# Kernel optimization log

Measured on AMD Instinct MI355X. Metric: run time of the kernel, lower is better.

Reference implementation:

```python
import jax, jax.numpy as jnp
import numpy as np

N, E, E_LG, H, KGE, NUM_GRAPHS, N_ITER = 100000, 500000, 1000000, 128, 128, 1024, 2
EPS = 1e-5

def _prelu(x, a):
    return jnp.where(x >= 0, x, a * x)

def _seg_mean(vals, idx, num):
    s = jax.ops.segment_sum(vals, idx, num_segments=num)
    c = jax.ops.segment_sum(jnp.ones((vals.shape[0],), vals.dtype), idx, num_segments=num)
    return s / jnp.maximum(c, 1.0)[:, None]

def setup_inputs() -> dict:
    key = jax.random.key(0)
    ks = jax.random.split(key, 16)
    sc = 1.0 / np.sqrt(H)
    inp = {
        "x": jax.random.normal(ks[0], (N, H), jnp.float32),
        "edge_attr": jax.random.normal(ks[1], (E, H), jnp.float32),
        "edge_index": jax.random.randint(ks[2], (2, E), 0, N),
        "batch": jnp.sort(jax.random.randint(ks[3], (N,), 0, NUM_GRAPHS)),
        "line_graph_edge_index": jax.random.randint(ks[4], (2, E_LG), 0, E),
        # edge_update_net: Linear + PReLU + BatchNorm1d (eval mode)
        "W1": jax.random.normal(ks[5], (H, H), jnp.float32) * sc,
        "b1": jnp.zeros((H,), jnp.float32),
        "a1": jnp.full((1,), 0.25, jnp.float32),
        "bn_gamma": jnp.ones((H,), jnp.float32),
        "bn_beta": jnp.zeros((H,), jnp.float32),
        "bn_mean": jnp.zeros((H,), jnp.float32),
        "bn_var": jnp.ones((H,), jnp.float32),
        # GRU (single layer, single step)
        "w_ih": jax.random.normal(ks[6], (3 * H, H), jnp.float32) * sc,
        "w_hh": jax.random.normal(ks[7], (3 * H, H), jnp.float32) * sc,
        "b_ih": jnp.zeros((3 * H,), jnp.float32),
        "b_hh": jnp.zeros((3 * H,), jnp.float32),
        # DynamicAttention net
        "Wa1": jax.random.normal(ks[8], (H // 2, H), jnp.float32) * sc,
        "ba1": jnp.zeros((H // 2,), jnp.float32),
        "a2": jnp.full((1,), 0.25, jnp.float32),
        "Wa2": jax.random.normal(ks[9], (1, H // 2), jnp.float32) * (1.0 / np.sqrt(H // 2)),
        "ba2": jnp.zeros((1,), jnp.float32),
        # readout
        "Wr": jax.random.normal(ks[10], (KGE, H), jnp.float32) * sc,
        "br": jnp.zeros((KGE,), jnp.float32),
    }
    return inp

def reference(x, edge_attr, W1, b1, a1, bn_gamma, bn_beta, bn_mean, bn_var,
              w_ih, w_hh, b_ih, b_hh, Wa1, ba1, a2, Wa2, ba2, Wr, br,
              edge_index, batch, line_graph_edge_index):
    src, dst = edge_index[0], edge_index[1]
    l_src, l_dst = line_graph_edge_index[0], line_graph_edge_index[1]
    h = x  # GRU hidden state [N, H]
    for _ in range(N_ITER):
        # edge-to-edge message passing (node_to_edge_proj is Identity here)
        fused = edge_attr + (x[src] + x[dst]) * 0.5  # [E, H]
        agg = _seg_mean(fused[l_src], l_dst, E)      # scatter-mean over line graph
        upd = _prelu(agg @ W1.T + b1, a1)
        upd = (upd - bn_mean) * jax.lax.rsqrt(bn_var + EPS) * bn_gamma + bn_beta
        fused = fused + upd
        node_updates = _seg_mean(fused, dst, N)      # [N, H]
        # single GRU step
        gi = node_updates @ w_ih.T + b_ih
        gh = h @ w_hh.T + b_hh
        gi_r, gi_z, gi_n = jnp.split(gi, 3, axis=-1)
        gh_r, gh_z, gh_n = jnp.split(gh, 3, axis=-1)
        r = jax.nn.sigmoid(gi_r + gh_r)
        z = jax.nn.sigmoid(gi_z + gh_z)
        n = jnp.tanh(gi_n + r * gh_n)
        h = (1.0 - z) * n + z * h
        x = h
    # dynamic attention: per-graph scalar gate
    graph_repr = _seg_mean(x, batch, NUM_GRAPHS)     # [G, H]
    attn = jax.nn.sigmoid(_prelu(graph_repr @ Wa1.T + ba1, a2) @ Wa2.T + ba2)  # [G, 1]
    attended = x * attn[batch]
    graph_emb = jax.ops.segment_sum(attended, batch, num_segments=NUM_GRAPHS)
    graph_emb = graph_emb @ Wr.T + br
    return (x, graph_emb)
```

## Files before the change

### kernel.cpp

```cpp
#include <hip/hip_runtime.h>
#include <stdint.h>

#define H 128
#define G_NUM 1024
#define BN_EPS 1e-5f

typedef unsigned int uint;
typedef unsigned short ushort;
typedef __attribute__((ext_vector_type(8))) __bf16 bf16x8;
typedef __attribute__((ext_vector_type(8))) ushort ushort8;
typedef __attribute__((ext_vector_type(4))) float f32x4;
typedef __attribute__((ext_vector_type(2))) float f32x2;

__device__ __forceinline__ float b2f(ushort u){ return __uint_as_float(((uint)u) << 16); }
__device__ __forceinline__ ushort f2b(float f){
    uint u = __float_as_uint(f);
    u += 0x7FFFu + ((u >> 16) & 1u);
    return (ushort)(u >> 16);
}
__device__ __forceinline__ float ldf(const void* p, size_t i, int bf){
    return bf ? b2f(((const ushort*)p)[i]) : ((const float*)p)[i];
}
__device__ __forceinline__ int swz(int r, int byte_in_row){
    return (r * 256 + byte_in_row) ^ ((r & 7) << 4);
}

__global__ void k_setup_small(const uint* __restrict__ gamma_bits,
                              const void* b1, const void* a1, const void* gam, const void* bet,
                              const void* mean, const void* var, const void* bih, const void* bhh,
                              float* __restrict__ ep, float* __restrict__ bi, float* __restrict__ bh,
                              int* __restrict__ flag, ushort* __restrict__ fz1, ushort* __restrict__ fz2,
                              size_t zoff, int* __restrict__ off_cat, int nk_idx, int sent_val){
    __shared__ int bfs;
    int t = threadIdx.x;
    if (t == 0){
        int f = (gamma_bits[0] == 0x3F803F80u) ? 1 : 0;
        *flag = f; bfs = f;
        off_cat[nk_idx] = sent_val;
    }
    __syncthreads();
    int bf = bfs;
    bi[t] = ldf(bih, t, bf);
    bh[t] = ldf(bhh, t, bf);
    if (t < 128){
        ep[t]       = ldf(b1, t, bf);
        ep[128 + t] = rsqrtf(ldf(var, t, bf) + BN_EPS) * ldf(gam, t, bf);
        ep[256 + t] = ldf(mean, t, bf);
        ep[384 + t] = ldf(bet, t, bf);
        fz1[zoff + t] = 0; fz2[zoff + t] = 0;
    }
    if (t == 0) ep[512] = ldf(a1, 0, bf);
}

__global__ __launch_bounds__(256) void k_count2(const int* __restrict__ lgi, const int* __restrict__ ei,
                                                int* __restrict__ cnt, int ELG, int E){
    int t = blockIdx.x * 256 + threadIdx.x;
    if (t < ELG) atomicAdd(&cnt[lgi[ELG + t]], 1);
    else { int t2 = t - ELG; if (t2 < E) atomicAdd(&cnt[E + ei[E + t2]], 1); }
}
__global__ __launch_bounds__(256) void k_scan_reduce(const int* __restrict__ cnt, int* __restrict__ bsum, int n){
    int base = blockIdx.x * 1024;
    int s = 0;
    for (int i = threadIdx.x; i < 1024; i += 256){ int idx = base + i; s += (idx < n) ? cnt[idx] : 0; }
    __shared__ int r[256];
    r[threadIdx.x] = s; __syncthreads();
    for (int o = 128; o > 0; o >>= 1){ if (threadIdx.x < o) r[threadIdx.x] += r[threadIdx.x + o]; __syncthreads(); }
    if (threadIdx.x == 0) bsum[blockIdx.x] = r[0];
}
__global__ __launch_bounds__(256) void k_scan_mid(int* __restrict__ bsum, int nb){
    __shared__ int ts[256];
    int tid = threadIdx.x;
    int loc[4]; int s = 0;
    #pragma unroll
    for (int j = 0; j < 4; j++){
        int idx = tid * 4 + j;
        loc[j] = s;
        s += (idx < nb) ? bsum[idx] : 0;
    }
    ts[tid] = s; __syncthreads();
    for (int o = 1; o < 256; o <<= 1){
        int v = (tid >= o) ? ts[tid - o] : 0;
        __syncthreads();
        ts[tid] += v;
        __syncthreads();
    }
    int texcl = ts[tid] - s;
    #pragma unroll
    for (int j = 0; j < 4; j++){
        int idx = tid * 4 + j;
        if (idx < nb) bsum[idx] = texcl + loc[j];
    }
}
__global__ __launch_bounds__(256) void k_scan_final(const int* __restrict__ cnt, const int* __restrict__ bsum,
                                                    int* __restrict__ off, int n){
    __shared__ int ts[256];
    int base = blockIdx.x * 1024;
    int tid = threadIdx.x;
    int loc[4]; int s = 0;
    #pragma unroll
    for (int j = 0; j < 4; j++){
        int idx = base + tid * 4 + j;
        loc[j] = s;
        s += (idx < n) ? cnt[idx] : 0;
    }
    ts[tid] = s; __syncthreads();
    for (int o = 1; o < 256; o <<= 1){
        int v = (tid >= o) ? ts[tid - o] : 0;
        __syncthreads();
        ts[tid] += v;
        __syncthreads();
    }
    int texcl = ts[tid] - s + bsum[blockIdx.x];
    #pragma unroll
    for (int j = 0; j < 4; j++){
        int idx = base + tid * 4 + j;
        if (idx < n) off[idx] = texcl + loc[j];
    }
}
__global__ __launch_bounds__(256) void k_fill2(const int* __restrict__ lgi, const int* __restrict__ ei,
                                               const int* __restrict__ off, int* __restrict__ cur,
                                               int* __restrict__ list, int ELG, int E){
    int t = blockIdx.x * 256 + threadIdx.x;
    if (t < ELG){
        int k = lgi[ELG + t];
        int pos = atomicAdd(&cur[k], 1);
        list[off[k] + pos] = lgi[t];
    } else {
        int t2 = t - ELG;
        if (t2 < E){
            int k = E + ei[E + t2];
            int pos = atomicAdd(&cur[k], 1);
            list[off[k] + pos] = t2;
        }
    }
}
__global__ __launch_bounds__(256) void k_cvt_bf(const void* __restrict__ in, ushort* __restrict__ out,
                                                int n, const int* __restrict__ flag){
    int t = blockIdx.x * 256 + threadIdx.x;
    if (t >= n) return;
    if (*flag) out[t] = ((const ushort*)in)[t];
    else       out[t] = f2b(((const float*)in)[t]);
}
__global__ __launch_bounds__(256) void k_wcvt(const void* __restrict__ W1, const void* __restrict__ wih,
                                              const void* __restrict__ whh, const void* __restrict__ Wr,
                                              ushort* __restrict__ W1bf, ushort* __restrict__ wihbf,
                                              ushort* __restrict__ whhbf, float* __restrict__ WrT,
                                              const int* __restrict__ flag){
    int t = blockIdx.x * 256 + threadIdx.x;
    int bf = *flag;
    if (t < 16384) W1bf[t] = bf ? ((const ushort*)W1)[t] : f2b(((const float*)W1)[t]);
    else if (t < 65536){ int i = t - 16384; wihbf[i] = bf ? ((const ushort*)wih)[i] : f2b(((const float*)wih)[i]); }
    else if (t < 114688){ int i = t - 65536; whhbf[i] = bf ? ((const ushort*)whh)[i] : f2b(((const float*)whh)[i]); }
    else if (t < 131072){ int i = t - 114688; int r = i >> 7, c = i & 127; WrT[c * 128 + r] = ldf(Wr, i, bf); }
}
__global__ __launch_bounds__(256) void k_store_h(const ushort* __restrict__ hb, void* __restrict__ out,
                                                 int n, const int* __restrict__ flag){
    int t = blockIdx.x * 256 + threadIdx.x;
    if (t >= n) return;
    ushort v = hb[t];
    if (*flag) ((ushort*)out)[t] = v;
    else       ((float*) out)[t] = b2f(v);
}

__global__ __launch_bounds__(256) void k_fused(const void* __restrict__ ea, const ushort* __restrict__ hb,
                                               const int* __restrict__ ei, ushort* __restrict__ fused,
                                               int E, const int* __restrict__ flag){
    int t = blockIdx.x * 256 + threadIdx.x;
    if (t >= E * 16) return;
    int bf = *flag;
    int e = t >> 4, ch = (t & 15) * 8;
    int s = ei[e], d = ei[E + e];
    ushort8 hs = *(const ushort8*)(hb + (size_t)s * H + ch);
    ushort8 hd = *(const ushort8*)(hb + (size_t)d * H + ch);
    size_t base = (size_t)e * H + ch;
    float av[8];
    if (bf){
        ushort8 a = *(const ushort8*)((const ushort*)ea + base);
        #pragma unroll
        for (int j = 0; j < 8; j++) av[j] = b2f(a[j]);
    } else {
        float4 a0 = *(const float4*)((const float*)ea + base);
        float4 a1 = *(const float4*)((const float*)ea + base + 4);
        av[0] = a0.x; av[1] = a0.y; av[2] = a0.z; av[3] = a0.w;
        av[4] = a1.x; av[5] = a1.y; av[6] = a1.z; av[7] = a1.w;
    }
    ushort8 o;
    #pragma unroll
    for (int j = 0; j < 8; j++) o[j] = f2b(av[j] + 0.5f * (b2f(hs[j]) + b2f(hd[j])));
    *(ushort8*)(fused + base) = o;
}

__global__ __launch_bounds__(256) void k_agg_gemm(const ushort* __restrict__ fused,
                                                  const int* __restrict__ off_cat, const int* __restrict__ list,
                                                  const ushort* __restrict__ W1bf, const float* __restrict__ ep,
                                                  ushort* __restrict__ fused2, int E, int LMAX){
    __shared__ __attribute__((aligned(16))) char As[32 * 256];
    __shared__ int offL[33];
    int tid = threadIdx.x, wid = tid >> 6, lane = tid & 63;
    int r0 = blockIdx.x * 32;
    if (tid < 33) offL[tid] = off_cat[r0 + tid];
    __syncthreads();
    int l16 = lane >> 4, ch16 = lane & 15;
    int rA = wid * 8 + l16, rB = rA + 4;
    int baseA = offL[rA], degA = offL[rA + 1] - baseA;
    int baseB = offL[rB], degB = offL[rB + 1] - baseB;
    int dm = max(degA, degB);
    #pragma unroll
    for (int o = 32; o > 0; o >>= 1) dm = max(dm, __shfl_xor(dm, o));
    f32x2 accA[4] = {}, accB[4] = {};
    #pragma unroll 2
    for (int i = 0; i < dm; i++){
        int liA = baseA + i; liA = (liA < LMAX) ? liA : (LMAX - 1);
        int liB = baseB + i; liB = (liB < LMAX) ? liB : (LMAX - 1);
        int sA = list[liA];
        int sB = list[liB];
        sA = (i < degA) ? sA : E;
        sB = (i < degB) ? sB : E;
        uint4 wA = *(const uint4*)(fused + (size_t)sA * H + ch16 * 8);
        uint4 wB = *(const uint4*)(fused + (size_t)sB * H + ch16 * 8);
        uint wa[4] = {wA.x, wA.y, wA.z, wA.w};
        uint wb[4] = {wB.x, wB.y, wB.z, wB.w};
        #pragma unroll
        for (int k2 = 0; k2 < 4; k2++){
            f32x2 va, vb;
            va.x = __uint_as_float(wa[k2] << 16); va.y = __uint_as_float(wa[k2] & 0xFFFF0000u);
            vb.x = __uint_as_float(wb[k2] << 16); vb.y = __uint_as_float(wb[k2] & 0xFFFF0000u);
            accA[k2] += va; accB[k2] += vb;
        }
    }
    float invA = 1.f / fmaxf((float)degA, 1.f);
    float invB = 1.f / fmaxf((float)degB, 1.f);
    ushort8 oA, oB;
    #pragma unroll
    for (int k2 = 0; k2 < 4; k2++){
        oA[2 * k2] = f2b(accA[k2].x * invA); oA[2 * k2 + 1] = f2b(accA[k2].y * invA);
        oB[2 * k2] = f2b(accB[k2].x * invB); oB[2 * k2 + 1] = f2b(accB[k2].y * invB);
    }
    *(ushort8*)(As + swz(rA, ch16 * 16)) = oA;
    *(ushort8*)(As + swz(rB, ch16 * 16)) = oB;
    __syncthreads();
    int lrow = lane & 15, lhi = lane >> 4;
    f32x4 acc[2][2] = {};
    #pragma unroll
    for (int ks = 0; ks < 4; ks++){
        bf16x8 afr[2];
        #pragma unroll
        for (int rt = 0; rt < 2; rt++)
            afr[rt] = *(const bf16x8*)(As + swz(rt * 16 + lrow, ks * 64 + lhi * 16));
        #pragma unroll
        for (int cc = 0; cc < 2; cc++){
            int c = (2 * wid + cc) * 16 + lrow;
            bf16x8 bfr = *(const bf16x8*)(W1bf + (size_t)c * H + ks * 32 + lhi * 8);
            #pragma unroll
            for (int rt = 0; rt < 2; rt++)
                acc[cc][rt] = __builtin_amdgcn_mfma_f32_16x16x32_bf16(afr[rt], bfr, acc[cc][rt], 0, 0, 0);
        }
    }
    __syncthreads();
    float aa = ep[512];
    #pragma unroll
    for (int cc = 0; cc < 2; cc++){
        int c = (2 * wid + cc) * 16 + lrow;
        float bb = ep[c], sc = ep[128 + c], mb = ep[256 + c], be = ep[384 + c];
        #pragma unroll
        for (int rt = 0; rt < 2; rt++)
            #pragma unroll
            for (int rg = 0; rg < 4; rg++){
                int r = rt * 16 + lhi * 4 + rg;
                float u = acc[cc][rt][rg] + bb;
                u = (u >= 0.f) ? u : aa * u;
                u = (u - mb) * sc + be;
                *(ushort*)(As + swz(r, c * 2)) = f2b(u);
            }
    }
    __syncthreads();
    #pragma unroll
    for (int q = 0; q < 2; q++){
        int r = (q == 0) ? rA : rB;
        size_t gbase = (size_t)(r0 + r) * H + ch16 * 8;
        ushort8 f = *(const ushort8*)(fused + gbase);
        ushort8 u = *(const ushort8*)(As + swz(r, ch16 * 16));
        ushort8 o;
        #pragma unroll
        for (int j = 0; j < 8; j++) o[j] = f2b(b2f(f[j]) + b2f(u[j]));
        *(ushort8*)(fused2 + gbase) = o;
    }
}

__global__ __launch_bounds__(256) void k_gru(const ushort* __restrict__ fused2,
                                             const int* __restrict__ off_cat, const int* __restrict__ list,
                                             ushort* __restrict__ hb,
                                             const ushort* __restrict__ wihbf, const ushort* __restrict__ whhbf,
                                             const float* __restrict__ bi, const float* __restrict__ bh,
                                             int N, int EZ, int LMAX){
    __shared__ __attribute__((aligned(16))) char NUs[32 * 256];
    __shared__ __attribute__((aligned(16))) char HHs[32 * 256];
    __shared__ int offL[33];
    int tid = threadIdx.x, wid = tid >> 6, lane = tid & 63;
    int r0 = blockIdx.x * 32;
    if (tid < 33) offL[tid] = off_cat[r0 + tid];
    int l16 = lane >> 4, ch16 = lane & 15;
    int rA = wid * 8 + l16, rB = rA + 4;
    *(ushort8*)(HHs + swz(rA, ch16 * 16)) = *(const ushort8*)(hb + (size_t)(r0 + rA) * H + ch16 * 8);
    *(ushort8*)(HHs + swz(rB, ch16 * 16)) = *(const ushort8*)(hb + (size_t)(r0 + rB) * H + ch16 * 8);
    __syncthreads();
    int baseA = offL[rA], degA = offL[rA + 1] - baseA;
    int baseB = offL[rB], degB = offL[rB + 1] - baseB;
    int dm = max(degA, degB);
    #pragma unroll
    for (int o = 32; o > 0; o >>= 1) dm = max(dm, __shfl_xor(dm, o));
    f32x2 accA[4] = {}, accB[4] = {};
    #pragma unroll 2
    for (int i = 0; i < dm; i++){
        int liA = baseA + i; liA = (liA < LMAX) ? liA : (LMAX - 1);
        int liB = baseB + i; liB = (liB < LMAX) ? liB : (LMAX - 1);
        int sA = list[liA];
        int sB = list[liB];
        sA = (i < degA) ? sA : EZ;
        sB = (i < degB) ? sB : EZ;
        uint4 wA = *(const uint4*)(fused2 + (size_t)sA * H + ch16 * 8);
        uint4 wB = *(const uint4*)(fused2 + (size_t)sB * H + ch16 * 8);
        uint wa[4] = {wA.x, wA.y, wA.z, wA.w};
        uint wb[4] = {wB.x, wB.y, wB.z, wB.w};
        #pragma unroll
        for (int k2 = 0; k2 < 4; k2++){
            f32x2 va, vb;
            va.x = __uint_as_float(wa[k2] << 16); va.y = __uint_as_float(wa[k2] & 0xFFFF0000u);
            vb.x = __uint_as_float(wb[k2] << 16); vb.y = __uint_as_float(wb[k2] & 0xFFFF0000u);
            accA[k2] += va; accB[k2] += vb;
        }
    }
    float invA = 1.f / fmaxf((float)degA, 1.f);
    float invB = 1.f / fmaxf((float)degB, 1.f);
    ushort8 oA, oB;
    #pragma unroll
    for (int k2 = 0; k2 < 4; k2++){
        oA[2 * k2] = f2b(accA[k2].x * invA); oA[2 * k2 + 1] = f2b(accA[k2].y * invA);
        oB[2 * k2] = f2b(accB[k2].x * invB); oB[2 * k2 + 1] = f2b(accB[k2].y * invB);
    }
    *(ushort8*)(NUs + swz(rA, ch16 * 16)) = oA;
    *(ushort8*)(NUs + swz(rB, ch16 * 16)) = oB;
    __syncthreads();
    int lrow = lane & 15, lhi = lane >> 4;
    ushort hnew[2][2][4];
    #pragma unroll
    for (int b = 0; b < 2; b++){
        f32x4 aI[3][2] = {}, aH[3][2] = {};
        #pragma unroll
        for (int ks = 0; ks < 4; ks++){
            bf16x8 fN[2], fH[2];
            #pragma unroll
            for (int rt = 0; rt < 2; rt++){
                int addr = swz(rt * 16 + lrow, ks * 64 + lhi * 16);
                fN[rt] = *(const bf16x8*)(NUs + addr);
                fH[rt] = *(const bf16x8*)(HHs + addr);
            }
            #pragma unroll
            for (int g = 0; g < 3; g++){
                int c = g * 128 + (wid + 4 * b) * 16 + lrow;
                bf16x8 bI = *(const bf16x8*)(wihbf + (size_t)c * H + ks * 32 + lhi * 8);
                bf16x8 bH = *(const bf16x8*)(whhbf + (size_t)c * H + ks * 32 + lhi * 8);
                #pragma unroll
                for (int rt = 0; rt < 2; rt++){
                    aI[g][rt] = __builtin_amdgcn_mfma_f32_16x16x32_bf16(fN[rt], bI, aI[g][rt], 0, 0, 0);
                    aH[g][rt] = __builtin_amdgcn_mfma_f32_16x16x32_bf16(fH[rt], bH, aH[g][rt], 0, 0, 0);
                }
            }
        }
        int c = (wid + 4 * b) * 16 + lrow;
        float bir = bi[c], biz = bi[128 + c], bin = bi[256 + c];
        float bhr = bh[c], bhz = bh[128 + c], bhn = bh[256 + c];
        #pragma unroll
        for (int rt = 0; rt < 2; rt++)
            #pragma unroll
            for (int rg = 0; rg < 4; rg++){
                int r = rt * 16 + lhi * 4 + rg;
                float gr = aI[0][rt][rg] + bir + aH[0][rt][rg] + bhr;
                float gz = aI[1][rt][rg] + biz + aH[1][rt][rg] + bhz;
                float rv = 1.f / (1.f + __expf(-gr));
                float zv = 1.f / (1.f + __expf(-gz));
                float nv = tanhf(aI[2][rt][rg] + bin + rv * (aH[2][rt][rg] + bhn));
                float hold = b2f(*(const ushort*)(HHs + swz(r, c * 2)));
                hnew[b][rt][rg] = f2b((1.f - zv) * nv + zv * hold);
            }
    }
    __syncthreads();
    #pragma unroll
    for (int b = 0; b < 2; b++){
        int c = (wid + 4 * b) * 16 + lrow;
        #pragma unroll
        for (int rt = 0; rt < 2; rt++)
            #pragma unroll
            for (int rg = 0; rg < 4; rg++){
                int r = rt * 16 + lhi * 4 + rg;
                *(ushort*)(NUs + swz(r, c * 2)) = hnew[b][rt][rg];
            }
    }
    __syncthreads();
    *(ushort8*)(hb + (size_t)(r0 + rA) * H + ch16 * 8) = *(const ushort8*)(NUs + swz(rA, ch16 * 16));
    *(ushort8*)(hb + (size_t)(r0 + rB) * H + ch16 * 8) = *(const ushort8*)(NUs + swz(rB, ch16 * 16));
}

__global__ __launch_bounds__(256) void k_gbounds(const int* __restrict__ batch, int* __restrict__ gs, int N, int G){
    int g = blockIdx.x * 256 + threadIdx.x;
    if (g > G) return;
    int lo = 0, hi = N;
    while (lo < hi){ int mid = (lo + hi) >> 1; if (batch[mid] < g) lo = mid + 1; else hi = mid; }
    gs[g] = lo;
}
__global__ __launch_bounds__(256) void k_graph_sum(const ushort* __restrict__ hb, const int* __restrict__ gs,
                                                   float* __restrict__ gsum){
    int g = blockIdx.x, c = threadIdx.x & 127, half = threadIdx.x >> 7;
    int s = gs[g], e = gs[g + 1];
    float acc0 = 0.f, acc1 = 0.f;
    int r = s + half;
    for (; r + 2 < e; r += 4){
        acc0 += b2f(hb[(size_t)r * H + c]);
        acc1 += b2f(hb[(size_t)(r + 2) * H + c]);
    }
    for (; r < e; r += 2) acc0 += b2f(hb[(size_t)r * H + c]);
    __shared__ float tmp[128];
    if (half == 1) tmp[c] = acc0 + acc1;
    __syncthreads();
    if (half == 0) gsum[(size_t)g * H + c] = acc0 + acc1 + tmp[c];
}
__global__ void k_attn(const float* __restrict__ gsum, const int* __restrict__ gs,
                       const void* __restrict__ Wa1, const void* __restrict__ ba1,
                       const void* __restrict__ a2, const void* __restrict__ Wa2,
                       const void* __restrict__ ba2, float* __restrict__ attn, const int* __restrict__ flag){
    int g = blockIdx.x;
    int j = threadIdx.x;
    int bf = *flag;
    float inv = 1.0f / fmaxf((float)(gs[g + 1] - gs[g]), 1.0f);
    __shared__ float R[H];
    for (int i = j; i < H; i += 64) R[i] = gsum[(size_t)g * H + i] * inv;
    __syncthreads();
    float t = 0.f;
    for (int k = 0; k < H; k++) t += R[k] * ldf(Wa1, (size_t)j * H + k, bf);
    t += ldf(ba1, j, bf);
    float al = ldf(a2, 0, bf);
    t = (t >= 0.f) ? t : al * t;
    float p = t * ldf(Wa2, j, bf);
    #pragma unroll
    for (int o = 32; o > 0; o >>= 1) p += __shfl_down(p, o);
    if (j == 0) attn[g] = 1.f / (1.f + __expf(-(p + ldf(ba2, 0, bf))));
}
__global__ __launch_bounds__(256) void k_graph_gemm(const float* __restrict__ gsum, const float* __restrict__ attn,
                                                    const float* __restrict__ WrT,
                                                    const void* __restrict__ br, void* __restrict__ out,
                                                    size_t obase, const int* __restrict__ flag){
    __shared__ float A[8 * H];
    int bf = *flag;
    int r0 = blockIdx.x * 8;
    for (int i = threadIdx.x; i < 8 * H; i += 256){
        int r = i >> 7;
        A[i] = gsum[(size_t)(r0 + r) * H + (i & 127)] * attn[r0 + r];
    }
    __syncthreads();
    int c = threadIdx.x & 127;
    int rr = (threadIdx.x >> 7) * 4;
    float acc[4] = {0, 0, 0, 0};
    for (int k = 0; k < H; k++){
        float w = WrT[k * H + c];
        #pragma unroll
        for (int j = 0; j < 4; j++) acc[j] += A[(rr + j) * H + k] * w;
    }
    float bb = ldf(br, c, bf);
    for (int j = 0; j < 4; j++){
        size_t idx = obase + (size_t)(r0 + rr + j) * H + c;
        float v = acc[j] + bb;
        if (bf) ((ushort*)out)[idx] = f2b(v);
        else    ((float*) out)[idx] = v;
    }
}

extern "C" void kernel_launch(void* const* d_in, const int* in_sizes, int n_in,
                              void* d_out, int out_size, void* d_ws, size_t ws_size,
                              hipStream_t stream)
{
    const void* x    = d_in[0];
    const void* ea   = d_in[1];
    const int*  ei   = (const int*)d_in[2];
    const int*  batch= (const int*)d_in[3];
    const int*  lgi  = (const int*)d_in[4];
    const void* W1   = d_in[5];
    const void* b1   = d_in[6];
    const void* a1   = d_in[7];
    const void* bng  = d_in[8];
    const void* bnb  = d_in[9];
    const void* bnm  = d_in[10];
    const void* bnv  = d_in[11];
    const void* wih  = d_in[12];
    const void* whh  = d_in[13];
    const void* bih  = d_in[14];
    const void* bhh  = d_in[15];
    const void* Wa1  = d_in[16];
    const void* ba1  = d_in[17];
    const void* a2   = d_in[18];
    const void* Wa2  = d_in[19];
    const void* ba2  = d_in[20];
    const void* Wr   = d_in[21];
    const void* br   = d_in[22];

    const int N   = in_sizes[0] / H;
    const int E   = in_sizes[1] / H;
    const int ELG = in_sizes[4] / 2;
    const int G   = G_NUM;
    const int NK  = E + N;
    const int nb  = (NK + 1023) / 1024;

    char* ws = (char*)d_ws;
    size_t off = 0;
    auto alloc = [&](size_t b) -> void* { void* p = ws + off; off += (b + 255) & ~(size_t)255; return p; };
    int*    flag    = (int*)   alloc(256);
    ushort* hb      = (ushort*)alloc((size_t)N * H * 2);
    ushort* fused   = (ushort*)alloc((size_t)(E + 1) * H * 2);
    ushort* fused2  = (ushort*)alloc((size_t)(E + 1) * H * 2);
    int*    zreg    = (int*)   alloc((size_t)(2 * NK) * 4);
    int*    cnt_cat = zreg;
    int*    cur_cat = zreg + NK;
    int*    off_cat = (int*)   alloc((size_t)(NK + 1) * 4);
    int*    list_cat= (int*)   alloc((size_t)(ELG + E) * 4);
    int*    bsum    = (int*)   alloc((size_t)(nb + 8) * 4);
    int*    gs      = (int*)   alloc((size_t)(G + 1) * 4);
    ushort* W1bf    = (ushort*)alloc(128 * 128 * 2);
    ushort* wihbf   = (ushort*)alloc(384 * 128 * 2);
    ushort* whhbf   = (ushort*)alloc(384 * 128 * 2);
    float*  ep      = (float*) alloc(513 * 4);
    float*  bi      = (float*) alloc(384 * 4);
    float*  bh      = (float*) alloc(384 * 4);
    float*  WrT     = (float*) alloc(128 * 128 * 4);
    float*  gsum    = (float*) alloc((size_t)G * H * 4);
    float*  attn    = (float*) alloc((size_t)G * 4);

    k_setup_small<<<1, 384, 0, stream>>>((const uint*)bng, b1, a1, bng, bnb, bnm, bnv, bih, bhh,
                                         ep, bi, bh, flag, fused, fused2, (size_t)E * H,
                                         off_cat, NK, ELG + E);

    hipMemsetAsync(zreg, 0, (size_t)(2 * NK) * 4, stream);
    k_count2<<<(ELG + E + 255) / 256, 256, 0, stream>>>(lgi, ei, cnt_cat, ELG, E);
    k_scan_reduce<<<nb, 256, 0, stream>>>(cnt_cat, bsum, NK);
    k_scan_mid<<<1, 256, 0, stream>>>(bsum, nb);
    k_scan_final<<<nb, 256, 0, stream>>>(cnt_cat, bsum, off_cat, NK);
    k_fill2<<<(ELG + E + 255) / 256, 256, 0, stream>>>(lgi, ei, off_cat, cur_cat, list_cat, ELG, E);

    k_wcvt<<<(131072 + 255) / 256, 256, 0, stream>>>(W1, wih, whh, Wr, W1bf, wihbf, whhbf, WrT, flag);

    k_cvt_bf<<<(N * H + 255) / 256, 256, 0, stream>>>(x, hb, N * H, flag);

    for (int it = 0; it < 2; it++){
        k_fused<<<(E * 16 + 255) / 256, 256, 0, stream>>>(ea, hb, ei, fused, E, flag);
        k_agg_gemm<<<(E + 31) / 32, 256, 0, stream>>>(fused, off_cat, list_cat, W1bf, ep, fused2, E, ELG);
        k_gru<<<(N + 31) / 32, 256, 0, stream>>>(fused2, off_cat + E, list_cat, hb, wihbf, whhbf, bi, bh, N, E, ELG + E);
    }

    k_gbounds<<<(G + 256) / 256, 256, 0, stream>>>(batch, gs, N, G);
    k_graph_sum<<<G, 256, 0, stream>>>(hb, gs, gsum);
    k_attn<<<G, 64, 0, stream>>>(gsum, gs, Wa1, ba1, a2, Wa2, ba2, attn, flag);
    k_graph_gemm<<<G / 8, 256, 0, stream>>>(gsum, attn, WrT, br, d_out, (size_t)N * H, flag);
    k_store_h<<<(N * H + 255) / 256, 256, 0, stream>>>(hb, d_out, N * H, flag);
}
```

Before: 965.4 us.

## Degree-sort rows within tiles to balance gather loops; fuse h store into graph sum

A new kernel bitonic-sorts each 32-row tile by in-degree into a byte permutation. The aggregation and GRU kernels use it so each wave handles rows of similar degree, which shrinks the wasted iterations from the per-wave max-degree loop. The GRU epilogue now writes new hidden values into a dedicated shared buffer, dropping one barrier and a register array. The separate final pass that stores h to the output is folded into the per-graph sum kernel, saving a full read of h. The costs are a small extra kernel, more shared memory in the GRU kernel, and an indirection load per row.

```diff
diff --git a/kernel.cpp b/kernel.cpp
--- a/kernel.cpp
+++ b/kernel.cpp
@@ -7,6 +7,7 @@
 
 typedef unsigned int uint;
 typedef unsigned short ushort;
+typedef unsigned char uchar;
 typedef __attribute__((ext_vector_type(8))) __bf16 bf16x8;
 typedef __attribute__((ext_vector_type(8))) ushort ushort8;
 typedef __attribute__((ext_vector_type(4))) float f32x4;
@@ -134,6 +135,29 @@
         }
     }
 }
+__global__ __launch_bounds__(256) void k_sortperm(const int* __restrict__ off, uchar* __restrict__ perm, int NK){
+    int t = blockIdx.x * 256 + threadIdx.x;
+    int wave = t >> 6;
+    int l = t & 63;
+    int l5 = l & 31;
+    int r0 = wave * 32;
+    if (r0 >= NK) return;
+    int r = r0 + l5;
+    int deg = off[r + 1] - off[r];
+    int key = (deg << 5) | l5;
+    #pragma unroll
+    for (int k = 2; k <= 32; k <<= 1){
+        #pragma unroll
+        for (int j = k >> 1; j > 0; j >>= 1){
+            int other = __shfl_xor(key, j);
+            bool dir = ((l5 & k) == 0);
+            bool lower = ((l5 & j) == 0);
+            int mn = min(key, other), mx = max(key, other);
+            key = (dir == lower) ? mn : mx;
+        }
+    }
+    if (l < 32) perm[r0 + l5] = (uchar)(key & 31);
+}
 __global__ __launch_bounds__(256) void k_cvt_bf(const void* __restrict__ in, ushort* __restrict__ out,
                                                 int n, const int* __restrict__ flag){
     int t = blockIdx.x * 256 + threadIdx.x;
@@ -152,14 +176,6 @@
     else if (t < 65536){ int i = t - 16384; wihbf[i] = bf ? ((const ushort*)wih)[i] : f2b(((const float*)wih)[i]); }
     else if (t < 114688){ int i = t - 65536; whhbf[i] = bf ? ((const ushort*)whh)[i] : f2b(((const float*)whh)[i]); }
     else if (t < 131072){ int i = t - 114688; int r = i >> 7, c = i & 127; WrT[c * 128 + r] = ldf(Wr, i, bf); }
-}
-__global__ __launch_bounds__(256) void k_store_h(const ushort* __restrict__ hb, void* __restrict__ out,
-                                                 int n, const int* __restrict__ flag){
-    int t = blockIdx.x * 256 + threadIdx.x;
-    if (t >= n) return;
-    ushort v = hb[t];
-    if (*flag) ((ushort*)out)[t] = v;
-    else       ((float*) out)[t] = b2f(v);
 }
 
 __global__ __launch_bounds__(256) void k_fused(const void* __restrict__ ea, const ushort* __restrict__ hb,
@@ -192,6 +208,7 @@
 
 __global__ __launch_bounds__(256) void k_agg_gemm(const ushort* __restrict__ fused,
                                                   const int* __restrict__ off_cat, const int* __restrict__ list,
+                                                  const uchar* __restrict__ perm,
                                                   const ushort* __restrict__ W1bf, const float* __restrict__ ep,
                                                   ushort* __restrict__ fused2, int E, int LMAX){
     __shared__ __attribute__((aligned(16))) char As[32 * 256];
@@ -202,8 +219,9 @@
     __syncthreads();
     int l16 = lane >> 4, ch16 = lane & 15;
     int rA = wid * 8 + l16, rB = rA + 4;
-    int baseA = offL[rA], degA = offL[rA + 1] - baseA;
-    int baseB = offL[rB], degB = offL[rB + 1] - baseB;
+    int plA = perm[r0 + rA], plB = perm[r0 + rB];
+    int baseA = offL[plA], degA = offL[plA + 1] - baseA;
+    int baseB = offL[plB], degB = offL[plB + 1] - baseB;
     int dm = max(degA, degB);
     #pragma unroll
     for (int o = 32; o > 0; o >>= 1) dm = max(dm, __shfl_xor(dm, o));
@@ -236,8 +254,8 @@
         oA[2 * k2] = f2b(accA[k2].x * invA); oA[2 * k2 + 1] = f2b(accA[k2].y * invA);
         oB[2 * k2] = f2b(accB[k2].x * invB); oB[2 * k2 + 1] = f2b(accB[k2].y * invB);
     }
-    *(ushort8*)(As + swz(rA, ch16 * 16)) = oA;
-    *(ushort8*)(As + swz(rB, ch16 * 16)) = oB;
+    *(ushort8*)(As + swz(plA, ch16 * 16)) = oA;
+    *(ushort8*)(As + swz(plB, ch16 * 16)) = oB;
     __syncthreads();
     int lrow = lane & 15, lhi = lane >> 4;
     f32x4 acc[2][2] = {};
@@ -289,12 +307,14 @@
 
 __global__ __launch_bounds__(256) void k_gru(const ushort* __restrict__ fused2,
                                              const int* __restrict__ off_cat, const int* __restrict__ list,
+                                             const uchar* __restrict__ perm,
                                              ushort* __restrict__ hb,
                                              const ushort* __restrict__ wihbf, const ushort* __restrict__ whhbf,
                                              const float* __restrict__ bi, const float* __restrict__ bh,
                                              int N, int EZ, int LMAX){
     __shared__ __attribute__((aligned(16))) char NUs[32 * 256];
     __shared__ __attribute__((aligned(16))) char HHs[32 * 256];
+    __shared__ __attribute__((aligned(16))) char HNs[32 * 256];
     __shared__ int offL[33];
     int tid = threadIdx.x, wid = tid >> 6, lane = tid & 63;
     int r0 = blockIdx.x * 32;
@@ -304,8 +324,9 @@
     *(ushort8*)(HHs + swz(rA, ch16 * 16)) = *(const ushort8*)(hb + (size_t)(r0 + rA) * H + ch16 * 8);
     *(ushort8*)(HHs + swz(rB, ch16 * 16)) = *(const ushort8*)(hb + (size_t)(r0 + rB) * H + ch16 * 8);
     __syncthreads();
-    int baseA = offL[rA], degA = offL[rA + 1] - baseA;
-    int baseB = offL[rB], degB = offL[rB + 1] - baseB;
+    int plA = perm[r0 + rA], plB = perm[r0 + rB];
+    int baseA = offL[plA], degA = offL[plA + 1] - baseA;
+    int baseB = offL[plB], degB = offL[plB + 1] - baseB;
     int dm = max(degA, degB);
     #pragma unroll
     for (int o = 32; o > 0; o >>= 1) dm = max(dm, __shfl_xor(dm, o));
@@ -338,12 +359,11 @@
         oA[2 * k2] = f2b(accA[k2].x * invA); oA[2 * k2 + 1] = f2b(accA[k2].y * invA);
         oB[2 * k2] = f2b(accB[k2].x * invB); oB[2 * k2 + 1] = f2b(accB[k2].y * invB);
     }
-    *(ushort8*)(NUs + swz(rA, ch16 * 16)) = oA;
-    *(ushort8*)(NUs + swz(rB, ch16 * 16)) = oB;
+    *(ushort8*)(NUs + swz(plA, ch16 * 16)) = oA;
+    *(ushort8*)(NUs + swz(plB, ch16 * 16)) = oB;
     __syncthreads();
     int lrow = lane & 15, lhi = lane >> 4;
-    ushort hnew[2][2][4];
-    #pragma unroll
+    #pragma unroll 1
     for (int b = 0; b < 2; b++){
         f32x4 aI[3][2] = {}, aH[3][2] = {};
         #pragma unroll
@@ -381,24 +401,12 @@
                 float zv = 1.f / (1.f + __expf(-gz));
                 float nv = tanhf(aI[2][rt][rg] + bin + rv * (aH[2][rt][rg] + bhn));
                 float hold = b2f(*(const ushort*)(HHs + swz(r, c * 2)));
-                hnew[b][rt][rg] = f2b((1.f - zv) * nv + zv * hold);
+                *(ushort*)(HNs + swz(r, c * 2)) = f2b((1.f - zv) * nv + zv * hold);
             }
     }
     __syncthreads();
-    #pragma unroll
-    for (int b = 0; b < 2; b++){
-        int c = (wid + 4 * b) * 16 + lrow;
-        #pragma unroll
-        for (int rt = 0; rt < 2; rt++)
-            #pragma unroll
-            for (int rg = 0; rg < 4; rg++){
-                int r = rt * 16 + lhi * 4 + rg;
-                *(ushort*)(NUs + swz(r, c * 2)) = hnew[b][rt][rg];
-            }
-    }
-    __syncthreads();
-    *(ushort8*)(hb + (size_t)(r0 + rA) * H + ch16 * 8) = *(const ushort8*)(NUs + swz(rA, ch16 * 16));
-    *(ushort8*)(hb + (size_t)(r0 + rB) * H + ch16 * 8) = *(const ushort8*)(NUs + swz(rB, ch16 * 16));
+    *(ushort8*)(hb + (size_t)(r0 + rA) * H + ch16 * 8) = *(const ushort8*)(HNs + swz(rA, ch16 * 16));
+    *(ushort8*)(hb + (size_t)(r0 + rB) * H + ch16 * 8) = *(const ushort8*)(HNs + swz(rB, ch16 * 16));
 }
 
 __global__ __launch_bounds__(256) void k_gbounds(const int* __restrict__ batch, int* __restrict__ gs, int N, int G){
@@ -409,16 +417,28 @@
     gs[g] = lo;
 }
 __global__ __launch_bounds__(256) void k_graph_sum(const ushort* __restrict__ hb, const int* __restrict__ gs,
-                                                   float* __restrict__ gsum){
+                                                   float* __restrict__ gsum, void* __restrict__ out,
+                                                   const int* __restrict__ flag){
     int g = blockIdx.x, c = threadIdx.x & 127, half = threadIdx.x >> 7;
+    int bf = *flag;
     int s = gs[g], e = gs[g + 1];
     float acc0 = 0.f, acc1 = 0.f;
     int r = s + half;
     for (; r + 2 < e; r += 4){
-        acc0 += b2f(hb[(size_t)r * H + c]);
-        acc1 += b2f(hb[(size_t)(r + 2) * H + c]);
-    }
-    for (; r < e; r += 2) acc0 += b2f(hb[(size_t)r * H + c]);
+        ushort u0 = hb[(size_t)r * H + c];
+        ushort u1 = hb[(size_t)(r + 2) * H + c];
+        float v0 = b2f(u0), v1 = b2f(u1);
+        acc0 += v0; acc1 += v1;
+        if (bf){ ((ushort*)out)[(size_t)r * H + c] = u0; ((ushort*)out)[(size_t)(r + 2) * H + c] = u1; }
+        else   { ((float*) out)[(size_t)r * H + c] = v0; ((float*) out)[(size_t)(r + 2) * H + c] = v1; }
+    }
+    for (; r < e; r += 2){
+        ushort u0 = hb[(size_t)r * H + c];
+        float v0 = b2f(u0);
+        acc0 += v0;
+        if (bf) ((ushort*)out)[(size_t)r * H + c] = u0;
+        else    ((float*) out)[(size_t)r * H + c] = v0;
+    }
     __shared__ float tmp[128];
     if (half == 1) tmp[c] = acc0 + acc1;
     __syncthreads();
@@ -521,6 +541,7 @@
     int*    cur_cat = zreg + NK;
     int*    off_cat = (int*)   alloc((size_t)(NK + 1) * 4);
     int*    list_cat= (int*)   alloc((size_t)(ELG + E) * 4);
+    uchar*  perm    = (uchar*) alloc((size_t)(NK + 32));
     int*    bsum    = (int*)   alloc((size_t)(nb + 8) * 4);
     int*    gs      = (int*)   alloc((size_t)(G + 1) * 4);
     ushort* W1bf    = (ushort*)alloc(128 * 128 * 2);
@@ -543,6 +564,7 @@
     k_scan_mid<<<1, 256, 0, stream>>>(bsum, nb);
     k_scan_final<<<nb, 256, 0, stream>>>(cnt_cat, bsum, off_cat, NK);
     k_fill2<<<(ELG + E + 255) / 256, 256, 0, stream>>>(lgi, ei, off_cat, cur_cat, list_cat, ELG, E);
+    k_sortperm<<<(NK / 32 * 64 + 255) / 256, 256, 0, stream>>>(off_cat, perm, NK);
 
     k_wcvt<<<(131072 + 255) / 256, 256, 0, stream>>>(W1, wih, whh, Wr, W1bf, wihbf, whhbf, WrT, flag);
 
@@ -550,13 +572,12 @@
 
     for (int it = 0; it < 2; it++){
         k_fused<<<(E * 16 + 255) / 256, 256, 0, stream>>>(ea, hb, ei, fused, E, flag);
-        k_agg_gemm<<<(E + 31) / 32, 256, 0, stream>>>(fused, off_cat, list_cat, W1bf, ep, fused2, E, ELG);
-        k_gru<<<(N + 31) / 32, 256, 0, stream>>>(fused2, off_cat + E, list_cat, hb, wihbf, whhbf, bi, bh, N, E, ELG + E);
+        k_agg_gemm<<<(E + 31) / 32, 256, 0, stream>>>(fused, off_cat, list_cat, perm, W1bf, ep, fused2, E, ELG);
+        k_gru<<<(N + 31) / 32, 256, 0, stream>>>(fused2, off_cat + E, list_cat, perm + E, hb, wihbf, whhbf, bi, bh, N, E, ELG + E);
     }
 
     k_gbounds<<<(G + 256) / 256, 256, 0, stream>>>(batch, gs, N, G);
-    k_graph_sum<<<G, 256, 0, stream>>>(hb, gs, gsum);
+    k_graph_sum<<<G, 256, 0, stream>>>(hb, gs, gsum, d_out, flag);
     k_attn<<<G, 64, 0, stream>>>(gsum, gs, Wa1, ba1, a2, Wa2, ba2, attn, flag);
     k_graph_gemm<<<G / 8, 256, 0, stream>>>(gsum, attn, WrT, br, d_out, (size_t)N * H, flag);
-    k_store_h<<<(N * H + 255) / 256, 256, 0, stream>>>(hb, d_out, N * H, flag);
-}
+}
```

Result: no change. 969.7 us (+0.4%).
